# Performance work log

Hardware: AMD Instinct MI355X
Metric: run time of the kernel (lower is better)

## Reference

```python
import jax, jax.numpy as jnp
import numpy as np

UNITS = 512
EMB = 256

def setup_inputs() -> dict:
    key = jax.random.key(0)
    ks = jax.random.split(key, 12)
    b, t = 64, 2048
    inputs = jax.random.normal(ks[0], (b, EMB), jnp.float32)
    h_tm1 = jax.random.normal(ks[1], (b, UNITS), jnp.float32)
    context = jax.random.normal(ks[2], (b, t, UNITS), jnp.float32)
    s = 0.02
    params = {
        "Wi": jax.random.normal(ks[3], (EMB, UNITS), jnp.float32) * s,
        "bi": jnp.zeros((UNITS,), jnp.float32),
        "kernel": jax.random.normal(ks[4], (UNITS, 3 * UNITS), jnp.float32) * s,
        "recurrent_kernel": jax.random.normal(ks[5], (UNITS, 3 * UNITS), jnp.float32) * s,
        "attention_kernel": jax.random.normal(ks[6], (UNITS, 3 * UNITS), jnp.float32) * s,
        "bias": jnp.zeros((3 * UNITS,), jnp.float32),
        "Wa": jax.random.normal(ks[7], (UNITS, UNITS), jnp.float32) * s,
        "ba_w": jnp.zeros((UNITS,), jnp.float32),
        "Ua": jax.random.normal(ks[8], (UNITS, UNITS), jnp.float32) * s,
        "ba_u": jnp.zeros((UNITS,), jnp.float32),
        "Va": jax.random.normal(ks[9], (UNITS, 1), jnp.float32) * s,
        "ba_v": jnp.zeros((1,), jnp.float32),
        "Wo": jax.random.normal(ks[10], (UNITS, UNITS), jnp.float32) * s,
        "bo": jnp.zeros((UNITS,), jnp.float32),
    }
    return {"inputs": inputs, "h_tm1": h_tm1, "context": context, **params}


def reference(inputs, h_tm1, context, Wi, bi, kernel, recurrent_kernel,
              attention_kernel, bias, Wa, ba_w, Ua, ba_u, Va, ba_v, Wo, bo):
    U = UNITS
    # input dense: embedding_size != units
    x = inputs @ Wi + bi                              # [b, U]
    # gate input projections (fused then split)
    xg = x @ kernel + bias                            # [b, 3U]
    x_z, x_r, x_h = xg[:, :U], xg[:, U:2*U], xg[:, 2*U:]
    # Bahdanau attention over context using h_tm1 as query
    score = jnp.tanh(context @ Wa + ba_w + (h_tm1 @ Ua + ba_u)[:, None, :])  # [b,t,U]
    score = score @ Va + ba_v                         # [b, t, 1]
    attn = jax.nn.softmax(score, axis=1)              # [b, t, 1]
    ctx_vec = jnp.sum(attn * context, axis=1)         # [b, U]
    cg = ctx_vec @ attention_kernel                   # [b, 3U]
    c_z, c_r, c_h = cg[:, :U], cg[:, U:2*U], cg[:, 2*U:]
    rec_z = h_tm1 @ recurrent_kernel[:, :U]
    rec_r = h_tm1 @ recurrent_kernel[:, U:2*U]
    z = jax.nn.sigmoid(x_z + rec_z + c_z)
    r = jax.nn.sigmoid(x_r + rec_r + c_r)
    rec_h = (r * h_tm1) @ recurrent_kernel[:, 2*U:]
    h_bar = jnp.tanh(x_h + rec_h + c_h)
    h = z * h_tm1 + (1.0 - z) * h_bar
    out = h @ Wo + bo
    return out, h
```

## Files before the change

kernel.cpp:

```cpp
#include <hip/hip_runtime.h>

#define UNITS 512
#define EMBD  256
#define BATCH 64
#define TLEN  2048

typedef __bf16 bf16x8 __attribute__((ext_vector_type(8)));
typedef float  f32x4  __attribute__((ext_vector_type(4)));

__device__ __forceinline__ unsigned short f2bf(float x) {
  return __builtin_bit_cast(unsigned short, (__bf16)x);
}
__device__ __forceinline__ float fast_tanh(float x) {
  float e = __expf(2.0f * x);
  return __fdividef(e - 1.0f, e + 1.0f);
}
__device__ __forceinline__ float fast_sigmoid(float x) {
  return __fdividef(1.0f, 1.0f + __expf(-x));
}

__device__ __forceinline__ void dot_core(const float* Asm, float (*red)[64],
                                         const float* __restrict__ Bm, int ldb,
                                         const float* __restrict__ b1,
                                         const float* __restrict__ b2,
                                         float* __restrict__ out, int ldo,
                                         int K, int bx, int m) {
  const int cl = threadIdx.x & 63;
  const int ks = threadIdx.x >> 6;
  const int c  = (bx << 6) + cl;
  const int kl = K >> 2;
  const float* bp = Bm + (size_t)(ks * kl) * ldb + c;
  float acc = 0.0f;
#pragma unroll 8
  for (int kk = 0; kk < kl; ++kk)
    acc = fmaf(Asm[ks * kl + kk], bp[(size_t)kk * ldb], acc);
  red[ks][cl] = acc;
  __syncthreads();
  if (threadIdx.x < 64) {
    int cc = (bx << 6) + threadIdx.x;
    float v = red[0][threadIdx.x] + red[1][threadIdx.x] +
              red[2][threadIdx.x] + red[3][threadIdx.x];
    if (b1) v += b1[cc];
    if (b2) v += b2[cc];
    out[(size_t)m * ldo + cc] = v;
  }
}

__global__ void stage1_kernel(const float* __restrict__ Wa,
                              unsigned short* __restrict__ WaF,
                              float* __restrict__ gO, float* __restrict__ gL,
                              const float* __restrict__ inputs,
                              const float* __restrict__ Wi,
                              const float* __restrict__ bi,
                              float* __restrict__ xbuf,
                              const float* __restrict__ h_tm1,
                              const float* __restrict__ Ua,
                              const float* __restrict__ ba_u,
                              const float* __restrict__ ba_w,
                              float* __restrict__ ubuf,
                              const float* __restrict__ rk,
                              float* __restrict__ rec_zr) {
  __shared__ float Asm[512];
  __shared__ float red[4][64];
  int bid = blockIdx.x;
  if (bid < 1024) {
    int idx = bid * 256 + threadIdx.x;
    int j  = idx & 7;
    int l  = (idx >> 3) & 63;
    int nt = (idx >> 9) & 31;
    int ks = idx >> 14;
    int k = ks * 32 + ((l >> 4) << 3) + j;
    int n = (nt << 4) + (l & 15);
    WaF[idx] = f2bf(Wa[k * 512 + n]);
    if (idx < BATCH * UNITS) gO[idx] = 0.0f;
    if (idx < BATCH)         gL[idx] = 0.0f;
    return;
  }
  bid -= 1024;
  if (bid < 512) {
    int bx = bid & 7, m = bid >> 3;
    for (int k = threadIdx.x; k < 256; k += 256) Asm[k] = inputs[m * 256 + k];
    __syncthreads();
    dot_core(Asm, red, Wi, 512, bi, nullptr, xbuf, 512, 256, bx, m);
    return;
  }
  bid -= 512;
  if (bid < 512) {
    int bx = bid & 7, m = bid >> 3;
    for (int k = threadIdx.x; k < 512; k += 256) Asm[k] = h_tm1[m * 512 + k];
    __syncthreads();
    dot_core(Asm, red, Ua, 512, ba_u, ba_w, ubuf, 512, 512, bx, m);
    return;
  }
  bid -= 512;
  {
    int bx = bid & 15, m = bid >> 4;
    for (int k = threadIdx.x; k < 512; k += 256) Asm[k] = h_tm1[m * 512 + k];
    __syncthreads();
    dot_core(Asm, red, rk, 1536, nullptr, nullptr, rec_zr, 1024, 512, bx, m);
  }
}

__global__ void xg_kernel(const float* __restrict__ xbuf,
                          const float* __restrict__ kern,
                          const float* __restrict__ bias,
                          float* __restrict__ xg) {
  __shared__ float Asm[512];
  __shared__ float red[4][64];
  int m = blockIdx.y;
  for (int k = threadIdx.x; k < 512; k += 256) Asm[k] = xbuf[m * 512 + k];
  __syncthreads();
  dot_core(Asm, red, kern, 1536, bias, nullptr, xg, 1536, 512, blockIdx.x, m);
}

__launch_bounds__(256, 2)
__global__ void score_ctx_kernel(const float* __restrict__ ctx,
                                 const unsigned short* __restrict__ WaF,
                                 const float* __restrict__ uvec,
                                 const float* __restrict__ Va,
                                 float* __restrict__ gO,
                                 float* __restrict__ gL) {
  __shared__ unsigned short As[2][64][40];
  __shared__ float sS[64];
  __shared__ float sE[64];

  const int b   = blockIdx.y;
  const int tc  = blockIdx.x;
  const int tid = threadIdx.x;
  const int lane  = tid & 63;
  const int w     = tid >> 6;
  const int row_a = lane & 15;
  const int kq    = lane >> 4;

  const float* ctile = ctx + ((size_t)b * TLEN + (size_t)tc * 64) * UNITS;

  if (tid < 64) sS[tid] = 0.0f;

  f32x4 acc[4][8];
#pragma unroll
  for (int mt = 0; mt < 4; ++mt)
#pragma unroll
    for (int nt = 0; nt < 8; ++nt)
      acc[mt][nt] = (f32x4){0.0f, 0.0f, 0.0f, 0.0f};

  const int r_st = tid & 63;
  const int half = tid >> 6;

  const float4* abase = (const float4*)(ctile + r_st * UNITS + half * 8);
  const bf16x8* bbase = (const bf16x8*)WaF + lane;

  float4 pa0[2], pa1[2];
  pa0[0] = abase[0]; pa0[1] = abase[1];
  pa1[0] = abase[8]; pa1[1] = abase[9];

  bf16x8 bcur[8], bnxt[8];
#pragma unroll
  for (int nt = 0; nt < 8; ++nt)
    bcur[nt] = bbase[(size_t)((w << 3) + nt) * 64];

  {
    ushort4 q0 = make_ushort4(f2bf(pa0[0].x), f2bf(pa0[0].y), f2bf(pa0[0].z), f2bf(pa0[0].w));
    ushort4 q1 = make_ushort4(f2bf(pa0[1].x), f2bf(pa0[1].y), f2bf(pa0[1].z), f2bf(pa0[1].w));
    *(ushort4*)&As[0][r_st][half * 8]     = q0;
    *(ushort4*)&As[0][r_st][half * 8 + 4] = q1;
  }

#pragma unroll
  for (int ks = 0; ks < 16; ++ks) {
    const int cur = ks & 1;
    __syncthreads();
    bf16x8 af[4];
#pragma unroll
    for (int mt = 0; mt < 4; ++mt)
      af[mt] = *(const bf16x8*)&As[cur][mt * 16 + row_a][kq * 8];
    if (ks < 14) {
      float4* pdst = (cur == 0) ? pa0 : pa1;
      pdst[0] = abase[(ks + 2) * 8];
      pdst[1] = abase[(ks + 2) * 8 + 1];
    }
    if (ks < 15) {
#pragma unroll
      for (int nt = 0; nt < 8; ++nt)
        bnxt[nt] = bbase[(size_t)((ks + 1) * 32 + (w << 3) + nt) * 64];
    }
#pragma unroll
    for (int nt = 0; nt < 8; ++nt)
#pragma unroll
      for (int mt = 0; mt < 4; ++mt)
        acc[mt][nt] = __builtin_amdgcn_mfma_f32_16x16x32_bf16(af[mt], bcur[nt], acc[mt][nt], 0, 0, 0);
    if (ks < 15) {
      const float4* psrc = (cur == 0) ? pa1 : pa0;
      ushort4 q0 = make_ushort4(f2bf(psrc[0].x), f2bf(psrc[0].y), f2bf(psrc[0].z), f2bf(psrc[0].w));
      ushort4 q1 = make_ushort4(f2bf(psrc[1].x), f2bf(psrc[1].y), f2bf(psrc[1].z), f2bf(psrc[1].w));
      *(ushort4*)&As[1 - cur][r_st][half * 8]     = q0;
      *(ushort4*)&As[1 - cur][r_st][half * 8 + 4] = q1;
#pragma unroll
      for (int nt = 0; nt < 8; ++nt) bcur[nt] = bnxt[nt];
    }
  }

  float uvals[8], vvals[8];
#pragma unroll
  for (int nt = 0; nt < 8; ++nt) {
    int n_g = (w << 7) + (nt << 4) + row_a;
    uvals[nt] = uvec[b * UNITS + n_g];
    vvals[nt] = Va[n_g];
  }
#pragma unroll
  for (int mt = 0; mt < 4; ++mt) {
#pragma unroll
    for (int r = 0; r < 4; ++r) {
      float v = 0.0f;
#pragma unroll
      for (int nt = 0; nt < 8; ++nt)
        v += fast_tanh(acc[mt][nt][r] + uvals[nt]) * vvals[nt];
      v += __shfl_xor(v, 1);
      v += __shfl_xor(v, 2);
      v += __shfl_xor(v, 4);
      v += __shfl_xor(v, 8);
      if (row_a == 0) atomicAdd(&sS[mt * 16 + kq * 4 + r], v);
    }
  }
  __syncthreads();
  if (tid < 64) sE[tid] = __expf(sS[tid]);
  __syncthreads();
  if (tid < 64) {
    float e = sE[tid];
#pragma unroll
    for (int off = 1; off < 64; off <<= 1) e += __shfl_xor(e, off);
    if (tid == 0) atomicAdd(&gL[b], e);
  }
#pragma unroll
  for (int cc = 0; cc < 2; ++cc) {
    int c = cc * 256 + tid;
    float o = 0.0f;
#pragma unroll 8
    for (int t = 0; t < 64; ++t)
      o = fmaf(sE[t], ctile[t * UNITS + c], o);
    atomicAdd(&gO[b * UNITS + c], o);
  }
}

__global__ void cg_kernel(const float* __restrict__ gO,
                          const float* __restrict__ gL,
                          const float* __restrict__ ak,
                          float* __restrict__ cg) {
  __shared__ float Asm[512];
  __shared__ float red[4][64];
  int m = blockIdx.y;
  float sc = __fdividef(1.0f, gL[m]);
  for (int k = threadIdx.x; k < 512; k += 256) Asm[k] = gO[m * 512 + k] * sc;
  __syncthreads();
  dot_core(Asm, red, ak, 1536, nullptr, nullptr, cg, 1536, 512, blockIdx.x, m);
}

__global__ void rech_kernel(const float* __restrict__ xg,
                            const float* __restrict__ reczr,
                            const float* __restrict__ cg,
                            const float* __restrict__ h,
                            const float* __restrict__ rkh,
                            float* __restrict__ out) {
  __shared__ float Asm[512];
  __shared__ float red[4][64];
  int m = blockIdx.y;
  for (int k = threadIdx.x; k < 512; k += 256) {
    float r = fast_sigmoid(xg[m * 1536 + 512 + k] + reczr[m * 1024 + 512 + k] +
                           cg[m * 1536 + 512 + k]);
    Asm[k] = r * h[m * 512 + k];
  }
  __syncthreads();
  dot_core(Asm, red, rkh, 1536, nullptr, nullptr, out, 512, 512, blockIdx.x, m);
}

__global__ void out_kernel(const float* __restrict__ xg,
                           const float* __restrict__ reczr,
                           const float* __restrict__ cg,
                           const float* __restrict__ rech,
                           const float* __restrict__ h_tm1,
                           const float* __restrict__ Wo,
                           const float* __restrict__ bo,
                           float* __restrict__ out,
                           float* __restrict__ hout) {
  __shared__ float Asm[512];
  __shared__ float red[4][64];
  int m = blockIdx.y;
  for (int k = threadIdx.x; k < 512; k += 256) {
    float z  = fast_sigmoid(xg[m * 1536 + k] + reczr[m * 1024 + k] + cg[m * 1536 + k]);
    float hb = fast_tanh(xg[m * 1536 + 1024 + k] + rech[m * 512 + k] +
                         cg[m * 1536 + 1024 + k]);
    float hn = z * h_tm1[m * 512 + k] + (1.0f - z) * hb;
    Asm[k] = hn;
    if (blockIdx.x == 0) hout[m * 512 + k] = hn;
  }
  __syncthreads();
  dot_core(Asm, red, Wo, 512, bo, nullptr, out, 512, 512, blockIdx.x, m);
}

extern "C" void kernel_launch(void* const* d_in, const int* in_sizes, int n_in,
                              void* d_out, int out_size, void* d_ws, size_t ws_size,
                              hipStream_t stream) {
  (void)in_sizes; (void)n_in; (void)out_size; (void)ws_size;
  const float* inputs = (const float*)d_in[0];
  const float* h_tm1  = (const float*)d_in[1];
  const float* ctx    = (const float*)d_in[2];
  const float* Wi     = (const float*)d_in[3];
  const float* bi     = (const float*)d_in[4];
  const float* kern   = (const float*)d_in[5];
  const float* rk     = (const float*)d_in[6];
  const float* ak     = (const float*)d_in[7];
  const float* bias   = (const float*)d_in[8];
  const float* Wa     = (const float*)d_in[9];
  const float* ba_w   = (const float*)d_in[10];
  const float* Ua     = (const float*)d_in[11];
  const float* ba_u   = (const float*)d_in[12];
  const float* Va     = (const float*)d_in[13];
  const float* Wo     = (const float*)d_in[15];
  const float* bo     = (const float*)d_in[16];

  float* out = (float*)d_out;
  float* ws  = (float*)d_ws;
  unsigned short* WaF = (unsigned short*)ws;
  float* gO     = ws + 131072;
  float* gL     = ws + 163840;
  float* xbuf   = ws + 163904;
  float* xg     = ws + 196672;
  float* ubuf   = ws + 294976;
  float* rec_zr = ws + 327744;
  float* cg     = ws + 393280;
  float* rech   = ws + 491584;

  stage1_kernel<<<3072, 256, 0, stream>>>(Wa, WaF, gO, gL,
                                          inputs, Wi, bi, xbuf,
                                          h_tm1, Ua, ba_u, ba_w, ubuf,
                                          rk, rec_zr);
  xg_kernel<<<dim3(24, 64), 256, 0, stream>>>(xbuf, kern, bias, xg);
  score_ctx_kernel<<<dim3(32, 64), 256, 0, stream>>>(ctx, WaF, ubuf, Va, gO, gL);
  cg_kernel<<<dim3(24, 64), 256, 0, stream>>>(gO, gL, ak, cg);
  rech_kernel<<<dim3(8, 64), 256, 0, stream>>>(xg, rec_zr, cg, h_tm1, rk + 1024, rech);
  out_kernel<<<dim3(8, 64), 256, 0, stream>>>(xg, rec_zr, cg, rech, h_tm1, Wo, bo,
                                              out, out + BATCH * UNITS);
}
```

Before: 543.0 us.

## Stage whole context tile in LDS up front, drop per-k double buffering

The score kernel now loads the entire 64x512 context tile into LDS as bf16 with fully coalesced float4 reads and a single barrier, instead of streaming 32-wide k-slices through a double-buffered LDS pipeline with a barrier per step. The B operand is loaded per k-step without register prefetch, and the MFMA block is wrapped in s_setprio to favour matrix issue. The Wa repack also switches to coalesced reads of Wa with scattered writes. In exchange, LDS use grows to about 66KB per block, which may lower occupancy, and the global-load latency is no longer overlapped with MFMA inside a block.

```diff
diff --git a/kernel.cpp b/kernel.cpp
--- a/kernel.cpp
+++ b/kernel.cpp
@@ -64,16 +64,18 @@
   __shared__ float red[4][64];
   int bid = blockIdx.x;
   if (bid < 1024) {
-    int idx = bid * 256 + threadIdx.x;
-    int j  = idx & 7;
-    int l  = (idx >> 3) & 63;
-    int nt = (idx >> 9) & 31;
-    int ks = idx >> 14;
-    int k = ks * 32 + ((l >> 4) << 3) + j;
-    int n = (nt << 4) + (l & 15);
-    WaF[idx] = f2bf(Wa[k * 512 + n]);
-    if (idx < BATCH * UNITS) gO[idx] = 0.0f;
-    if (idx < BATCH)         gL[idx] = 0.0f;
+    int flat = bid * 256 + threadIdx.x;
+    int k = flat >> 9;
+    int n = flat & 511;
+    int ks = k >> 5;
+    int hi = (k >> 3) & 3;
+    int j  = k & 7;
+    int l  = (hi << 4) | (n & 15);
+    int nt = n >> 4;
+    int idx = (ks << 14) | (nt << 9) | (l << 3) | j;
+    WaF[idx] = f2bf(Wa[flat]);
+    if (flat < BATCH * UNITS) gO[flat] = 0.0f;
+    if (flat < BATCH)         gL[flat] = 0.0f;
     return;
   }
   bid -= 1024;
@@ -120,7 +122,7 @@
                                  const float* __restrict__ Va,
                                  float* __restrict__ gO,
                                  float* __restrict__ gL) {
-  __shared__ unsigned short As[2][64][40];
+  __shared__ unsigned short As[64][520];
   __shared__ float sS[64];
   __shared__ float sE[64];
 
@@ -143,60 +145,37 @@
     for (int nt = 0; nt < 8; ++nt)
       acc[mt][nt] = (f32x4){0.0f, 0.0f, 0.0f, 0.0f};
 
-  const int r_st = tid & 63;
-  const int half = tid >> 6;
-
-  const float4* abase = (const float4*)(ctile + r_st * UNITS + half * 8);
+  {
+    const float4* cbase = (const float4*)ctile;
+    const int rbase = tid >> 7;
+    const int kk    = (tid & 127) * 4;
+#pragma unroll 8
+    for (int j = 0; j < 32; ++j) {
+      float4 v = cbase[j * 256 + tid];
+      ushort4 q = make_ushort4(f2bf(v.x), f2bf(v.y), f2bf(v.z), f2bf(v.w));
+      *(ushort4*)&As[2 * j + rbase][kk] = q;
+    }
+  }
+  __syncthreads();
+
   const bf16x8* bbase = (const bf16x8*)WaF + lane;
-
-  float4 pa0[2], pa1[2];
-  pa0[0] = abase[0]; pa0[1] = abase[1];
-  pa1[0] = abase[8]; pa1[1] = abase[9];
-
-  bf16x8 bcur[8], bnxt[8];
-#pragma unroll
-  for (int nt = 0; nt < 8; ++nt)
-    bcur[nt] = bbase[(size_t)((w << 3) + nt) * 64];
-
-  {
-    ushort4 q0 = make_ushort4(f2bf(pa0[0].x), f2bf(pa0[0].y), f2bf(pa0[0].z), f2bf(pa0[0].w));
-    ushort4 q1 = make_ushort4(f2bf(pa0[1].x), f2bf(pa0[1].y), f2bf(pa0[1].z), f2bf(pa0[1].w));
-    *(ushort4*)&As[0][r_st][half * 8]     = q0;
-    *(ushort4*)&As[0][r_st][half * 8 + 4] = q1;
-  }
-
 #pragma unroll
   for (int ks = 0; ks < 16; ++ks) {
-    const int cur = ks & 1;
-    __syncthreads();
     bf16x8 af[4];
 #pragma unroll
     for (int mt = 0; mt < 4; ++mt)
-      af[mt] = *(const bf16x8*)&As[cur][mt * 16 + row_a][kq * 8];
-    if (ks < 14) {
-      float4* pdst = (cur == 0) ? pa0 : pa1;
-      pdst[0] = abase[(ks + 2) * 8];
-      pdst[1] = abase[(ks + 2) * 8 + 1];
-    }
-    if (ks < 15) {
-#pragma unroll
-      for (int nt = 0; nt < 8; ++nt)
-        bnxt[nt] = bbase[(size_t)((ks + 1) * 32 + (w << 3) + nt) * 64];
-    }
+      af[mt] = *(const bf16x8*)&As[mt * 16 + row_a][ks * 32 + kq * 8];
+    bf16x8 bf[8];
 #pragma unroll
     for (int nt = 0; nt < 8; ++nt)
+      bf[nt] = bbase[(size_t)(ks * 32 + (w << 3) + nt) * 64];
+    __builtin_amdgcn_s_setprio(1);
+#pragma unroll
+    for (int nt = 0; nt < 8; ++nt)
 #pragma unroll
       for (int mt = 0; mt < 4; ++mt)
-        acc[mt][nt] = __builtin_amdgcn_mfma_f32_16x16x32_bf16(af[mt], bcur[nt], acc[mt][nt], 0, 0, 0);
-    if (ks < 15) {
-      const float4* psrc = (cur == 0) ? pa1 : pa0;
-      ushort4 q0 = make_ushort4(f2bf(psrc[0].x), f2bf(psrc[0].y), f2bf(psrc[0].z), f2bf(psrc[0].w));
-      ushort4 q1 = make_ushort4(f2bf(psrc[1].x), f2bf(psrc[1].y), f2bf(psrc[1].z), f2bf(psrc[1].w));
-      *(ushort4*)&As[1 - cur][r_st][half * 8]     = q0;
-      *(ushort4*)&As[1 - cur][r_st][half * 8 + 4] = q1;
-#pragma unroll
-      for (int nt = 0; nt < 8; ++nt) bcur[nt] = bnxt[nt];
-    }
+        acc[mt][nt] = __builtin_amdgcn_mfma_f32_16x16x32_bf16(af[mt], bf[nt], acc[mt][nt], 0, 0, 0);
+    __builtin_amdgcn_s_setprio(0);
   }
 
   float uvals[8], vvals[8];
```

Result: no change. 533.9 us (-1.7%).
